# Performance work log

Measured on AMD Instinct MI355X. Metric: run time of the kernel, lower is better.

Reference implementation:

```python
import jax, jax.numpy as jnp
import numpy as np

B, N, P, T = 64, 200, 400, 1200
TOPK, STRIDE = 3, 25
THRESHOLD = 0.3  # args.threshold
EPS = 1e-9


def setup_inputs() -> dict:
    key = jax.random.key(0)
    k1, k2, k3 = jax.random.split(key, 3)
    x = jax.random.normal(k1, (B, N, T), jnp.float32)
    # xavier_uniform with gain=1.414 on (P, N) parameter
    limit = 1.414 * np.sqrt(6.0 / (P + N))
    patterns = jax.random.uniform(k2, (P, N), jnp.float32, -limit, limit)
    length = jax.random.randint(k3, (B,), 500, T + 1).astype(jnp.int32)
    return {"x": x, "patterns": patterns, "length": length}


def _forward(x, patterns, length):
    # size after temporal max-pool, per sample
    size_after_pool = jnp.floor(length.astype(jnp.float32) / STRIDE)  # (B,)

    # L2-normalize the learned patterns (P, N)
    normalized_patterns = patterns / jnp.sqrt((patterns ** 2).sum(-1, keepdims=True) + EPS)

    # top_select: keep top-K entries by |value| along node dim
    _, topi = jax.lax.top_k(jnp.abs(normalized_patterns), TOPK)  # (P, K)
    mask = jnp.zeros((P, N), jnp.float32).at[jnp.arange(P)[:, None], topi].set(1.0)
    toppattern = mask * normalized_patterns  # (P, N)

    # HCP_static branch: frames = x.transpose(2,1) -> (B, T, N)
    frames = x.transpose(0, 2, 1)
    normalized_frames = frames / jnp.sqrt((frames ** 2).sum(-1, keepdims=True) + EPS)

    # cosine similarity of every frame to every pattern: (B, T, P)
    sim = jnp.einsum('btn,pn->btp', normalized_frames, normalized_patterns)

    # non-overlapping max-pool over time with kernel=stride=STRIDE
    simw = sim.transpose(0, 2, 1).reshape(B, P, T // STRIDE, STRIDE)  # (B,P,Tp,S)
    posscores = simw.max(-1)          # (B, P, Tp)
    negscores = (-simw).max(-1)       # (B, P, Tp)
    sap = size_after_pool[:, None, None]
    compos = (posscores / sap).sum(-1)  # (B, P)
    comneg = (negscores / sap).sum(-1)  # (B, P)
    PES = (compos + comneg) / 2.0       # (B, P)

    # graphs = key_patterns.T @ diag(PES) @ key_patterns * non_diag_scale
    key_patterns = jax.lax.stop_gradient(toppattern)  # detach
    c = TOPK * P / N
    non_diag_scale = jnp.full((N, N), c, jnp.float32) - jnp.eye(N, dtype=jnp.float32) * (c - 1.0)
    graphs = jnp.einsum('pn,bp,pm->bnm', key_patterns, PES, key_patterns) * non_diag_scale

    # SigLoss(normalized_patterns, toppattern)
    lenp = jnp.linalg.norm(normalized_patterns, axis=-1)
    lentopp = jnp.linalg.norm(toppattern, axis=-1)
    norm = ((1.0 - lentopp / lenp) ** 2).mean()

    # Relaxed_orthloss(normalized_patterns, threshold)
    simpp = (normalized_patterns @ normalized_patterns.T) * (1.0 - jnp.eye(P, dtype=jnp.float32))
    orth = (jax.nn.relu((jnp.abs(simpp) - THRESHOLD) / (1.0 - THRESHOLD + 1e-5)) ** 2).mean()

    return graphs, norm, orth


def reference(x, patterns, length):
    return _forward(x, patterns, length)
```

## Files before the change

kernel.cpp:

```cpp
#include <hip/hip_runtime.h>
#include <math.h>

#define B_ 64
#define N_ 200
#define P_ 400
#define T_ 1200
#define TPAD 1280
#define PPAD 512
#define STRIDE_ 25
#define EPS_ 1e-9f
#define KPAD 224
#define BSTRIDE 232

#define OFF_NPATT  0
#define OFF_NPB16  80000
#define OFF_KEYVAL 124800
#define OFF_KEYIDX 126400
#define OFF_PES    128000
#define OFF_NORMB  153600
#define OFF_ORTHB  153700
#define OFF_NORM   OFF_NORMB
#define OFF_ORTH   OFF_ORTHB
#define OFF_NPBT   153728
#define OFF_XN     211072
#define OFF_GPOOL  9386112
#define WS_FAST_FLOATS (9386112 + 2457600)

#define PAT_BLKS 100
#define TN_BLKS  (20 * B_)
#define ZG_BLKS  40
#define ZP_BLKS  2
#define ZO_BLKS  160
#define PREP_BLKS (PAT_BLKS + TN_BLKS + ZG_BLKS + ZP_BLKS + ZO_BLKS)

typedef float f4v __attribute__((ext_vector_type(4)));
typedef short s8v __attribute__((ext_vector_type(8)));

__device__ inline unsigned short f2bf(float f) {
    union { float f; unsigned u; } v; v.f = f;
    unsigned r = v.u + 0x7FFFu + ((v.u >> 16) & 1u);
    return (unsigned short)(r >> 16);
}
__device__ inline unsigned okey(float f) {
    unsigned u = __float_as_uint(f);
    return (u & 0x80000000u) ? ~u : (u | 0x80000000u);
}
__device__ inline float dekey(unsigned k) {
    unsigned u = (k & 0x80000000u) ? (k & 0x7fffffffu) : ~k;
    return __uint_as_float(u);
}

__device__ float pat_body(const float* __restrict__ patterns, float* __restrict__ ws,
                          int p, int lane) {
    float v0 = patterns[p * N_ + lane];
    float v1 = patterns[p * N_ + lane + 64];
    float v2 = patterns[p * N_ + lane + 128];
    float v3 = (lane < 8) ? patterns[p * N_ + lane + 192] : 0.0f;

    float ss = v0 * v0 + v1 * v1 + v2 * v2 + v3 * v3;
    for (int off = 32; off; off >>= 1) ss += __shfl_down(ss, off);
    ss = __shfl(ss, 0);

    float rn = 1.0f / sqrtf(ss + EPS_);
    float s0 = v0 * rn, s1 = v1 * rn, s2 = v2 * rn, s3 = v3 * rn;

    float* npatT = ws + OFF_NPATT;
    npatT[(lane) * P_ + p] = s0;
    npatT[(lane + 64) * P_ + p] = s1;
    npatT[(lane + 128) * P_ + p] = s2;
    if (lane < 8) npatT[(lane + 192) * P_ + p] = s3;

    unsigned short* npb = (unsigned short*)(ws + OFF_NPB16);
    unsigned short b0 = f2bf(s0), b1 = f2bf(s1), b2 = f2bf(s2), b3 = f2bf(s3);
    npb[p * KPAD + lane] = b0;
    npb[p * KPAD + lane + 64] = b1;
    npb[p * KPAD + lane + 128] = b2;
    if (lane < 8) npb[p * KPAD + lane + 192] = b3;
    if (lane < 24) npb[p * KPAD + 200 + lane] = 0;

    unsigned short* npbT = (unsigned short*)(ws + OFF_NPBT);
    {
        int k0 = lane, k1 = lane + 64, k2 = lane + 128;
        npbT[(k0 >> 3) * (PPAD * 8) + p * 8 + (k0 & 7)] = b0;
        npbT[(k1 >> 3) * (PPAD * 8) + p * 8 + (k1 & 7)] = b1;
        npbT[(k2 >> 3) * (PPAD * 8) + p * 8 + (k2 & 7)] = b2;
        if (lane < 8) {
            int k3 = lane + 192;
            npbT[(k3 >> 3) * (PPAD * 8) + p * 8 + (k3 & 7)] = b3;
        }
        if (lane < 24) {
            int k4 = 200 + lane;
            npbT[(k4 >> 3) * (PPAD * 8) + p * 8 + (k4 & 7)] = 0;
        }
    }

    float a0 = fabsf(s0), a1 = fabsf(s1), a2 = fabsf(s2), a3 = fabsf(s3);

    int ch0 = -1, ch1 = -1, ch2 = -1;
    float cs0 = 0.f, cs1 = 0.f, cs2 = 0.f;

    for (int r = 0; r < 3; r++) {
        float bv = -1.0f;
        int bi = 1 << 30;
        {
            int n = lane;
            bool sk = (n == ch0) || (n == ch1) || (n == ch2);
            if (!sk && a0 > bv) { bv = a0; bi = n; }
        }
        {
            int n = lane + 64;
            bool sk = (n == ch0) || (n == ch1) || (n == ch2);
            if (!sk && (a1 > bv || (a1 == bv && n < bi))) { bv = a1; bi = n; }
        }
        {
            int n = lane + 128;
            bool sk = (n == ch0) || (n == ch1) || (n == ch2);
            if (!sk && (a2 > bv || (a2 == bv && n < bi))) { bv = a2; bi = n; }
        }
        if (lane < 8) {
            int n = lane + 192;
            bool sk = (n == ch0) || (n == ch1) || (n == ch2);
            if (!sk && (a3 > bv || (a3 == bv && n < bi))) { bv = a3; bi = n; }
        }
        for (int off = 32; off; off >>= 1) {
            float ov = __shfl_down(bv, off);
            int oi = __shfl_down(bi, off);
            if (ov > bv || (ov == bv && oi < bi)) { bv = ov; bi = oi; }
        }
        bi = __shfl(bi, 0);
        int slot = bi >> 6, src = bi & 63;
        float mine = (slot == 0) ? s0 : (slot == 1) ? s1 : (slot == 2) ? s2 : s3;
        float sval = __shfl(mine, src);
        if (r == 0) { ch0 = bi; cs0 = sval; }
        else if (r == 1) { ch1 = bi; cs1 = sval; }
        else { ch2 = bi; cs2 = sval; }
    }

    float d2 = 0.f;
    if (lane == 0) {
        float* keyval = ws + OFF_KEYVAL;
        int* keyidx = (int*)(ws + OFF_KEYIDX);
        keyval[p * 4 + 0] = cs0; keyval[p * 4 + 1] = cs1; keyval[p * 4 + 2] = cs2;
        keyidx[p * 4 + 0] = ch0; keyidx[p * 4 + 1] = ch1; keyidx[p * 4 + 2] = ch2;
        float lenp = sqrtf(ss) * rn;
        float lentopp = sqrtf(cs0 * cs0 + cs1 * cs1 + cs2 * cs2);
        float d = 1.0f - lentopp / lenp;
        d2 = d * d * (1.0f / (float)P_);
    }
    return d2;
}

__global__ __launch_bounds__(256) void prep_kernel(const float* __restrict__ x,
                                                   const float* __restrict__ patterns,
                                                   float* __restrict__ ws,
                                                   float* __restrict__ out) {
    __shared__ float xt[64 * 210];
    __shared__ float psums[256];
    __shared__ float rns[64];
    __shared__ float sh4[4];

    const int tid = threadIdx.x;

    if (blockIdx.x < PAT_BLKS) {
        int wv = tid >> 6, lane = tid & 63;
        int p = blockIdx.x * 4 + wv;
        float d2 = pat_body(patterns, ws, p, lane);
        if (lane == 0) sh4[wv] = d2;
        __syncthreads();
        if (tid == 0)
            ws[OFF_NORMB + blockIdx.x] = sh4[0] + sh4[1] + sh4[2] + sh4[3];
        return;
    }
    if (blockIdx.x >= PAT_BLKS + TN_BLKS) {
        int zb = blockIdx.x - PAT_BLKS - TN_BLKS;
        if (zb < ZG_BLKS) {
            uint4* gp4 = (uint4*)(ws + OFF_GPOOL);
            int base = zb * 15360 + tid;
#pragma unroll
            for (int i = 0; i < 60; ++i)
                gp4[base + i * 256] = make_uint4(0, 0, 0, 0);
        } else if (zb < ZG_BLKS + ZP_BLKS) {
            unsigned* p32 = (unsigned*)(ws + OFF_NPBT);
            int lb = zb - ZG_BLKS;
            for (int e = lb * 256 + tid; e < 12544; e += ZP_BLKS * 256) {
                int seg = e / 448, r32 = e % 448;
                p32[seg * 2048 + 1600 + r32] = 0u;
            }
        } else {
            int zo = zb - ZG_BLKS - ZP_BLKS;
            uint4* o4 = (uint4*)out;
            for (int i = zo * 256 + tid; i < 640000; i += ZO_BLKS * 256)
                o4[i] = make_uint4(0, 0, 0, 0);
        }
        return;
    }

    const int blk = blockIdx.x - PAT_BLKS;
    const int t = tid & 63, r = tid >> 6;
    const int b = blk / 20;
    const int t0 = (blk % 20) * 64;
    const bool valid = (t0 + t) < T_;

    float ss = 0.0f;
    if (valid) {
        const float* xp = x + (size_t)b * N_ * T_ + t0 + t;
#pragma unroll 5
        for (int i = 0; i < 50; ++i) {
            int n = r * 50 + i;
            float v = xp[(size_t)n * T_];
            ss += v * v;
            xt[t * 210 + n] = v;
        }
    }
    psums[tid] = ss;
    __syncthreads();
    if (tid < 64) {
        float s = psums[tid] + psums[tid + 64] + psums[tid + 128] + psums[tid + 192];
        rns[tid] = rsqrtf(s + EPS_);
    }
    __syncthreads();

    unsigned short* xnT = (unsigned short*)(ws + OFF_XN);
#pragma unroll
    for (int j = 0; j < 7; ++j) {
        int idx = tid + 256 * j;
        int seg = idx >> 6, tt = idx & 63;
        s8v ov = (s8v){0, 0, 0, 0, 0, 0, 0, 0};
        if (seg < 25 && (t0 + tt) < T_) {
            float rn = rns[tt];
            const float* src = &xt[tt * 210 + seg * 8];
            unsigned o[4];
#pragma unroll
            for (int i = 0; i < 4; ++i)
                o[i] = (unsigned)f2bf(src[2 * i] * rn) |
                       ((unsigned)f2bf(src[2 * i + 1] * rn) << 16);
            ov = (s8v){(short)(o[0] & 0xffff), (short)(o[0] >> 16),
                       (short)(o[1] & 0xffff), (short)(o[1] >> 16),
                       (short)(o[2] & 0xffff), (short)(o[2] >> 16),
                       (short)(o[3] & 0xffff), (short)(o[3] >> 16)};
        }
        *(s8v*)(xnT + (((size_t)b * 28 + seg) * TPAD + t0 + tt) * 8) = ov;
    }
}

__global__ __launch_bounds__(256, 4) void work_kernel(float* __restrict__ ws,
                                                      unsigned* __restrict__ gpool) {
    __shared__ short ldsB[80 * BSTRIDE];
    __shared__ unsigned pool[2 * 7 * 80];

    const int tid = threadIdx.x;
    int orig = blockIdx.x;
    int xcd = orig & 7, rem = orig >> 3;
    int nid = (xcd < 4 ? xcd * 83 : 4 * 83 + (xcd - 4) * 82) + rem;

    const bool isOrth = (nid >= 640);
    int pb, mbg, b;
    if (isOrth) { int o = nid - 640; pb = o % 5; mbg = o / 5; b = 0; }
    else        { pb = nid % 5; mbg = (nid / 5) % 2; b = nid / 10; }

    const unsigned short* npb = (const unsigned short*)(ws + OFF_NPB16) + (size_t)(pb * 80) * KPAD;

#pragma unroll
    for (int j = 0; j < 9; ++j) {
        int idx = tid + 256 * j;
        if (idx < 2240) {
            int row = idx / 28, seg = idx % 28;
            *(s8v*)(&ldsB[row * BSTRIDE + seg * 8]) = *(const s8v*)(npb + (size_t)row * KPAD + seg * 8);
        }
    }
    for (int i = tid; i < 1120; i += 256) pool[i] = 0u;
    __syncthreads();

    const int wv = tid >> 6;
    const int lane = tid & 63;
    const int l15 = lane & 15, kg = lane >> 4;

    const int ROWS = isOrth ? PPAD : TPAD;
    const unsigned short* abase = isOrth
        ? (const unsigned short*)(ws + OFF_NPBT)
        : (const unsigned short*)(ws + OFF_XN) + (size_t)b * 28 * TPAD * 8;
    const int segstep = 4 * ROWS * 8;
    const int niter = isOrth ? 1 : 5;

    float orthpart = 0.f;

    for (int it = 0; it < niter; ++it) {
        const int mb = isOrth ? mbg : (mbg * 5 + it);
        const int row0 = mb * 128 + wv * 32 + l15;
        const unsigned short* ar0 = abase + ((size_t)kg * ROWS + row0) * 8;
        const unsigned short* ar1 = ar0 + 16 * 8;

        f4v acc[2][5];
#pragma unroll
        for (int mi = 0; mi < 2; ++mi)
#pragma unroll
            for (int ni = 0; ni < 5; ++ni) acc[mi][ni] = (f4v){0.f, 0.f, 0.f, 0.f};

        s8v A[4][2];
#pragma unroll
        for (int c = 0; c < 4; ++c) {
            A[c][0] = *(const s8v*)(ar0 + c * segstep);
            A[c][1] = *(const s8v*)(ar1 + c * segstep);
        }

#pragma unroll
        for (int c = 0; c < 7; ++c) {
            if (c + 4 < 7) {
                A[(c + 4) & 3][0] = *(const s8v*)(ar0 + (c + 4) * segstep);
                A[(c + 4) & 3][1] = *(const s8v*)(ar1 + (c + 4) * segstep);
            }
            s8v bf[5];
#pragma unroll
            for (int ni = 0; ni < 5; ++ni)
                bf[ni] = *(const s8v*)(&ldsB[(ni * 16 + l15) * BSTRIDE + c * 32 + kg * 8]);
#pragma unroll
            for (int ni = 0; ni < 5; ++ni) {
                acc[0][ni] = __builtin_amdgcn_mfma_f32_16x16x32_bf16(A[c & 3][0], bf[ni], acc[0][ni], 0, 0, 0);
                acc[1][ni] = __builtin_amdgcn_mfma_f32_16x16x32_bf16(A[c & 3][1], bf[ni], acc[1][ni], 0, 0, 0);
            }
        }

        if (isOrth) {
#pragma unroll
            for (int mi = 0; mi < 2; ++mi) {
                int rb = mb * 128 + wv * 32 + mi * 16 + kg * 4;
#pragma unroll
                for (int ni = 0; ni < 5; ++ni) {
                    int col = pb * 80 + ni * 16 + l15;
#pragma unroll
                    for (int jj = 0; jj < 4; ++jj) {
                        if (rb + jj == col) continue;
                        float t = (fabsf(acc[mi][ni][jj]) - 0.3f) * (1.0f / 0.70001f);
                        if (t > 0.0f) orthpart += t * t;
                    }
                }
            }
            break;
        }

        const int wbase = (mb * 128) / 25;
#pragma unroll
        for (int mi = 0; mi < 2; ++mi) {
            int f0 = mb * 128 + wv * 32 + mi * 16 + kg * 4;
            int w0 = f0 / 25, w3 = (f0 + 3) / 25;
            int wsplit = w3 * 25;
#pragma unroll
            for (int ni = 0; ni < 5; ++ni) {
                int pc = ni * 16 + l15;
                float p0 = -1e30f, p1 = -1e30f, n0 = -1e30f, n1 = -1e30f;
#pragma unroll
                for (int jj = 0; jj < 4; ++jj) {
                    float v = acc[mi][ni][jj];
                    if (f0 + jj < wsplit) { p0 = fmaxf(p0, v); n0 = fmaxf(n0, -v); }
                    else                 { p1 = fmaxf(p1, v); n1 = fmaxf(n1, -v); }
                }
                atomicMax(&pool[(0 * 7 + (w3 - wbase)) * 80 + pc], okey(p1));
                atomicMax(&pool[(1 * 7 + (w3 - wbase)) * 80 + pc], okey(n1));
                if (w0 != w3) {
                    atomicMax(&pool[(0 * 7 + (w0 - wbase)) * 80 + pc], okey(p0));
                    atomicMax(&pool[(1 * 7 + (w0 - wbase)) * 80 + pc], okey(n0));
                }
            }
        }
        __syncthreads();
        for (int e = tid; e < 1120; e += 256) {
            unsigned v = pool[e];
            pool[e] = 0u;
            if (!v) continue;
            int pass = e / 560, r2 = e % 560;
            int w = wbase + r2 / 80, p = r2 % 80;
            if (w < 48)
                atomicMax(&gpool[((size_t)(pass * B_ + b) * 48 + w) * 400 + pb * 80 + p], v);
        }
        __syncthreads();
    }

    if (isOrth) {
        for (int off = 32; off; off >>= 1) orthpart += __shfl_down(orthpart, off);
        __syncthreads();
        float* red = (float*)pool;
        if (lane == 0) red[wv] = orthpart;
        __syncthreads();
        if (tid == 0)
            ws[OFF_ORTHB + (nid - 640)] = (red[0] + red[1] + red[2] + red[3]) *
                                          (1.0f / ((float)P_ * (float)P_));
    }
}

__global__ __launch_bounds__(256) void graphs_kernel(const unsigned* __restrict__ gpool,
                                                     const int* __restrict__ length,
                                                     const float* __restrict__ ws,
                                                     float* __restrict__ out) {
    int idx = blockIdx.x * 256 + threadIdx.x;
    if (idx == 0) {
        float sn = 0.f;
        for (int i = 0; i < PAT_BLKS; ++i) sn += ws[OFF_NORMB + i];
        out[(size_t)B_ * N_ * N_] = sn;
        float so = 0.f;
        for (int i = 0; i < 20; ++i) so += ws[OFF_ORTHB + i];
        out[(size_t)B_ * N_ * N_ + 1] = so;
    }
    if (idx >= B_ * P_) return;
    int b = idx / P_;
    int p = idx - b * P_;

    const unsigned* gp0 = gpool + (size_t)b * 48 * 400 + p;
    const unsigned* gp1 = gpool + (size_t)(B_ + b) * 48 * 400 + p;
    float s = 0.f;
#pragma unroll
    for (int w = 0; w < 48; ++w)
        s += dekey(gp0[w * 400]) + dekey(gp1[w * 400]);
    float rsap = 1.0f / (float)(length[b] / STRIDE_);
    float e = s * 0.5f * rsap;

    const float* keyval = ws + OFF_KEYVAL;
    const int* keyidx = (const int*)(ws + OFF_KEYIDX);
    float va[3] = { keyval[p * 4 + 0], keyval[p * 4 + 1], keyval[p * 4 + 2] };
    int ia[3] = { keyidx[p * 4 + 0], keyidx[p * 4 + 1], keyidx[p * 4 + 2] };

    float* g = out + (size_t)b * N_ * N_;
#pragma unroll
    for (int a = 0; a < 3; a++) {
#pragma unroll
        for (int c = 0; c < 3; c++) {
            float scale = (ia[a] == ia[c]) ? 1.0f : 6.0f;
            atomicAdd(&g[ia[a] * N_ + ia[c]], va[a] * va[c] * e * scale);
        }
    }
}

__global__ __launch_bounds__(256) void main_kernel(const float* __restrict__ x,
                                                   const int* __restrict__ length,
                                                   const float* __restrict__ ws,
                                                   float* __restrict__ pes) {
    __shared__ float xs[N_][STRIDE_ + 1];
    __shared__ float rnorm[STRIDE_];
    __shared__ float poolp[P_][5];
    __shared__ float pooln[P_][5];

    int w = blockIdx.x;
    int b = blockIdx.y;
    const float* xb = x + (size_t)b * N_ * T_ + (size_t)w * STRIDE_;

    for (int i = threadIdx.x; i < N_ * STRIDE_; i += 256) {
        int n = i / STRIDE_;
        int t = i - n * STRIDE_;
        xs[n][t] = xb[n * T_ + t];
    }
    __syncthreads();

    if (threadIdx.x < STRIDE_) {
        float ssf = 0.0f;
        for (int n = 0; n < N_; n++) { float vv = xs[n][threadIdx.x]; ssf += vv * vv; }
        rnorm[threadIdx.x] = 1.0f / sqrtf(ssf + EPS_);
    }
    __syncthreads();

    int pt = threadIdx.x % 50;
    int tt = threadIdx.x / 50;

    if (tt < 5) {
        float acc[8][5];
#pragma unroll
        for (int i = 0; i < 8; i++)
#pragma unroll
            for (int j = 0; j < 5; j++) acc[i][j] = 0.0f;

        const float4* np4 = (const float4*)(ws + OFF_NPATT);
        int pbq = pt * 2;
        for (int n = 0; n < N_; n++) {
            float4 q0 = np4[n * (P_ / 4) + pbq];
            float4 q1 = np4[n * (P_ / 4) + pbq + 1];
            float qa[8] = { q0.x, q0.y, q0.z, q0.w, q1.x, q1.y, q1.z, q1.w };
            float xv0 = xs[n][tt * 5 + 0];
            float xv1 = xs[n][tt * 5 + 1];
            float xv2 = xs[n][tt * 5 + 2];
            float xv3 = xs[n][tt * 5 + 3];
            float xv4 = xs[n][tt * 5 + 4];
#pragma unroll
            for (int i = 0; i < 8; i++) {
                acc[i][0] += qa[i] * xv0;
                acc[i][1] += qa[i] * xv1;
                acc[i][2] += qa[i] * xv2;
                acc[i][3] += qa[i] * xv3;
                acc[i][4] += qa[i] * xv4;
            }
        }
#pragma unroll
        for (int i = 0; i < 8; i++) {
            float pm = -1e30f, nm = -1e30f;
#pragma unroll
            for (int j = 0; j < 5; j++) {
                float s = acc[i][j] * rnorm[tt * 5 + j];
                pm = fmaxf(pm, s);
                nm = fmaxf(nm, -s);
            }
            poolp[pt * 8 + i][tt] = pm;
            pooln[pt * 8 + i][tt] = nm;
        }
    }
    __syncthreads();

    float rsap = 1.0f / (float)(length[b] / STRIDE_);
    for (int p = threadIdx.x; p < P_; p += 256) {
        float pm = poolp[p][0], nm = pooln[p][0];
#pragma unroll
        for (int q = 1; q < 5; q++) {
            pm = fmaxf(pm, poolp[p][q]);
            nm = fmaxf(nm, pooln[p][q]);
        }
        atomicAdd(&pes[b * P_ + p], (pm + nm) * 0.5f * rsap);
    }
}

__global__ __launch_bounds__(256) void fb_graphs_kernel(const float* __restrict__ ws,
                                                        float* __restrict__ out) {
    int idx = blockIdx.x * 256 + threadIdx.x;
    if (idx == 0) {
        out[(size_t)B_ * N_ * N_] = ws[OFF_NORM];
        out[(size_t)B_ * N_ * N_ + 1] = ws[OFF_ORTH];
    }
    if (idx >= B_ * P_) return;
    int b = idx / P_;
    int p = idx - b * P_;
    float e = ws[OFF_PES + b * P_ + p];
    const float* keyval = ws + OFF_KEYVAL;
    const int* keyidx = (const int*)(ws + OFF_KEYIDX);
    float va[3] = { keyval[p * 4 + 0], keyval[p * 4 + 1], keyval[p * 4 + 2] };
    int ia[3] = { keyidx[p * 4 + 0], keyidx[p * 4 + 1], keyidx[p * 4 + 2] };
    float* g = out + (size_t)b * N_ * N_;
#pragma unroll
    for (int a = 0; a < 3; a++)
#pragma unroll
        for (int c = 0; c < 3; c++) {
            float scale = (ia[a] == ia[c]) ? 1.0f : 6.0f;
            atomicAdd(&g[ia[a] * N_ + ia[c]], va[a] * va[c] * e * scale);
        }
}

__global__ __launch_bounds__(64) void pat_kernel(const float* __restrict__ patterns,
                                                 float* __restrict__ ws) {
    float d2 = pat_body(patterns, ws, blockIdx.x, threadIdx.x & 63);
    if (threadIdx.x == 0) atomicAdd(ws + OFF_NORM, d2);
}
__global__ __launch_bounds__(256) void orth_kernel(float* __restrict__ ws) {
    __shared__ float rowi[N_];
    __shared__ float red[256];
    const float* npatT = ws + OFF_NPATT;
    int i = blockIdx.x;
    for (int k = threadIdx.x; k < N_; k += 256) rowi[k] = npatT[k * P_ + i];
    __syncthreads();
    float partial = 0.0f;
    for (int j = threadIdx.x; j < P_; j += 256) {
        if (j == i) continue;
        float s = 0.0f;
        for (int k = 0; k < N_; k++) s += rowi[k] * npatT[k * P_ + j];
        float t = (fabsf(s) - 0.3f) * (1.0f / 0.70001f);
        if (t > 0.0f) partial += t * t;
    }
    red[threadIdx.x] = partial;
    __syncthreads();
    for (int sft = 128; sft; sft >>= 1) {
        if (threadIdx.x < sft) red[threadIdx.x] += red[threadIdx.x + sft];
        __syncthreads();
    }
    if (threadIdx.x == 0)
        atomicAdd(ws + OFF_ORTH, red[0] * (1.0f / ((float)P_ * (float)P_)));
}

extern "C" void kernel_launch(void* const* d_in, const int* in_sizes, int n_in,
                              void* d_out, int out_size, void* d_ws, size_t ws_size,
                              hipStream_t stream) {
    const float* x = (const float*)d_in[0];
    const float* patterns = (const float*)d_in[1];
    const int* length = (const int*)d_in[2];
    float* out = (float*)d_out;
    float* ws = (float*)d_ws;

    if (ws_size >= (size_t)WS_FAST_FLOATS * sizeof(float)) {
        unsigned* gpool = (unsigned*)(ws + OFF_GPOOL);
        prep_kernel<<<PREP_BLKS, 256, 0, stream>>>(x, patterns, ws, out);
        work_kernel<<<660, 256, 0, stream>>>(ws, gpool);
        graphs_kernel<<<(B_ * P_ + 255) / 256, 256, 0, stream>>>(gpool, length, ws, out);
    } else {
        hipMemsetAsync(d_out, 0, (size_t)B_ * N_ * N_ * sizeof(float), stream);
        hipMemsetAsync(ws + OFF_PES, 0, (size_t)(B_ * P_) * sizeof(float), stream);
        hipMemsetAsync(ws + OFF_NORM, 0, sizeof(float), stream);
        hipMemsetAsync(ws + OFF_ORTH, 0, sizeof(float), stream);
        pat_kernel<<<P_, 64, 0, stream>>>(patterns, ws);
        orth_kernel<<<P_, 256, 0, stream>>>(ws);
        main_kernel<<<dim3(T_ / STRIDE_, B_), 256, 0, stream>>>(x, length, ws, ws + OFF_PES);
        fb_graphs_kernel<<<(B_ * P_ + 255) / 256, 256, 0, stream>>>(ws, out);
    }
}
```

Baseline: 77.72 us.

## Store transposed x tile as bf16 in LDS and dispatch zeroing blocks first

The prep kernel's transpose tile in shared memory now holds bf16 values instead of fp32, halving LDS use so more blocks can be resident per CU. The zero-fill blocks for output and workspace are reordered to come first in the grid, ahead of the pattern and transpose blocks. The bf16 staging adds a second rounding step (value rounded to bf16, then scaled, then rounded again), which slightly changes numerics.

New measurement: 75.53 us. 1.03x faster.

```diff
diff --git a/kernel.cpp b/kernel.cpp
--- a/kernel.cpp
+++ b/kernel.cpp
@@ -26,12 +26,13 @@
 #define OFF_GPOOL  9386112
 #define WS_FAST_FLOATS (9386112 + 2457600)
 
+#define ZO_BLKS  160
+#define ZG_BLKS  40
+#define ZP_BLKS  2
 #define PAT_BLKS 100
 #define TN_BLKS  (20 * B_)
-#define ZG_BLKS  40
-#define ZP_BLKS  2
-#define ZO_BLKS  160
-#define PREP_BLKS (PAT_BLKS + TN_BLKS + ZG_BLKS + ZP_BLKS + ZO_BLKS)
+#define Z_ALL    (ZO_BLKS + ZG_BLKS + ZP_BLKS)
+#define PREP_BLKS (Z_ALL + PAT_BLKS + TN_BLKS)
 
 typedef float f4v __attribute__((ext_vector_type(4)));
 typedef short s8v __attribute__((ext_vector_type(8)));
@@ -154,48 +155,49 @@
                                                    const float* __restrict__ patterns,
                                                    float* __restrict__ ws,
                                                    float* __restrict__ out) {
-    __shared__ float xt[64 * 210];
+    __shared__ unsigned short xt16[64 * 210];
     __shared__ float psums[256];
     __shared__ float rns[64];
     __shared__ float sh4[4];
 
     const int tid = threadIdx.x;
 
-    if (blockIdx.x < PAT_BLKS) {
+    if (blockIdx.x < Z_ALL) {
+        int zb = blockIdx.x;
+        if (zb < ZO_BLKS) {
+            uint4* o4 = (uint4*)out;
+            for (int i = zb * 256 + tid; i < 640000; i += ZO_BLKS * 256)
+                o4[i] = make_uint4(0, 0, 0, 0);
+        } else if (zb < ZO_BLKS + ZG_BLKS) {
+            uint4* gp4 = (uint4*)(ws + OFF_GPOOL);
+            int base = (zb - ZO_BLKS) * 15360 + tid;
+#pragma unroll
+            for (int i = 0; i < 60; ++i)
+                gp4[base + i * 256] = make_uint4(0, 0, 0, 0);
+        } else {
+            unsigned* p32 = (unsigned*)(ws + OFF_NPBT);
+            int lb = zb - ZO_BLKS - ZG_BLKS;
+            for (int e = lb * 256 + tid; e < 12544; e += ZP_BLKS * 256) {
+                int seg = e / 448, r32 = e % 448;
+                p32[seg * 2048 + 1600 + r32] = 0u;
+            }
+        }
+        return;
+    }
+
+    if (blockIdx.x < Z_ALL + PAT_BLKS) {
+        int pblk = blockIdx.x - Z_ALL;
         int wv = tid >> 6, lane = tid & 63;
-        int p = blockIdx.x * 4 + wv;
+        int p = pblk * 4 + wv;
         float d2 = pat_body(patterns, ws, p, lane);
         if (lane == 0) sh4[wv] = d2;
         __syncthreads();
         if (tid == 0)
-            ws[OFF_NORMB + blockIdx.x] = sh4[0] + sh4[1] + sh4[2] + sh4[3];
+            ws[OFF_NORMB + pblk] = sh4[0] + sh4[1] + sh4[2] + sh4[3];
         return;
     }
-    if (blockIdx.x >= PAT_BLKS + TN_BLKS) {
-        int zb = blockIdx.x - PAT_BLKS - TN_BLKS;
-        if (zb < ZG_BLKS) {
-            uint4* gp4 = (uint4*)(ws + OFF_GPOOL);
-            int base = zb * 15360 + tid;
-#pragma unroll
-            for (int i = 0; i < 60; ++i)
-                gp4[base + i * 256] = make_uint4(0, 0, 0, 0);
-        } else if (zb < ZG_BLKS + ZP_BLKS) {
-            unsigned* p32 = (unsigned*)(ws + OFF_NPBT);
-            int lb = zb - ZG_BLKS;
-            for (int e = lb * 256 + tid; e < 12544; e += ZP_BLKS * 256) {
-                int seg = e / 448, r32 = e % 448;
-                p32[seg * 2048 + 1600 + r32] = 0u;
-            }
-        } else {
-            int zo = zb - ZG_BLKS - ZP_BLKS;
-            uint4* o4 = (uint4*)out;
-            for (int i = zo * 256 + tid; i < 640000; i += ZO_BLKS * 256)
-                o4[i] = make_uint4(0, 0, 0, 0);
-        }
-        return;
-    }
-
-    const int blk = blockIdx.x - PAT_BLKS;
+
+    const int blk = blockIdx.x - Z_ALL - PAT_BLKS;
     const int t = tid & 63, r = tid >> 6;
     const int b = blk / 20;
     const int t0 = (blk % 20) * 64;
@@ -209,7 +211,7 @@
             int n = r * 50 + i;
             float v = xp[(size_t)n * T_];
             ss += v * v;
-            xt[t * 210 + n] = v;
+            xt16[t * 210 + n] = f2bf(v);
         }
     }
     psums[tid] = ss;
@@ -228,12 +230,15 @@
         s8v ov = (s8v){0, 0, 0, 0, 0, 0, 0, 0};
         if (seg < 25 && (t0 + tt) < T_) {
             float rn = rns[tt];
-            const float* src = &xt[tt * 210 + seg * 8];
+            const unsigned* src = (const unsigned*)&xt16[tt * 210 + seg * 8];
             unsigned o[4];
 #pragma unroll
-            for (int i = 0; i < 4; ++i)
-                o[i] = (unsigned)f2bf(src[2 * i] * rn) |
-                       ((unsigned)f2bf(src[2 * i + 1] * rn) << 16);
+            for (int i = 0; i < 4; ++i) {
+                unsigned u = src[i];
+                float lo = __uint_as_float(u << 16) * rn;
+                float hi = __uint_as_float(u & 0xffff0000u) * rn;
+                o[i] = (unsigned)f2bf(lo) | ((unsigned)f2bf(hi) << 16);
+            }
             ov = (s8v){(short)(o[0] & 0xffff), (short)(o[0] >> 16),
                        (short)(o[1] & 0xffff), (short)(o[1] >> 16),
                        (short)(o[2] & 0xffff), (short)(o[2] >> 16),
```
